# Optimization experiments

Measured on AMD Instinct MI355X. Metric: run time of the kernel, lower is better.

Reference implementation:

```python
import jax, jax.numpy as jnp
import numpy as np

BATCH, N_PRE, N_POST = 1024, 8192, 8192
DT = 0.001
TAU_SYN = 0.005
SYN_NOISE_STD = 0.15
ALPHA_SYN = float(np.exp(-DT / TAU_SYN))  # exp(-dt/tau_syn) decay buffer


def setup_inputs() -> dict:
    key = jax.random.key(0)
    ks = jax.random.split(key, 6)
    spikes = jax.random.uniform(ks[0], (BATCH, N_PRE), dtype=jnp.float32)
    I_syn = jax.random.normal(ks[1], (BATCH, N_POST), dtype=jnp.float32) * 1e-10
    x_std = jax.random.uniform(ks[2], (BATCH, N_PRE), dtype=jnp.float32)
    noise = jax.random.normal(ks[3], (BATCH, N_POST), dtype=jnp.float32)
    # synapse counts from connectome -> norm_counts * mask (precomputed buffer)
    counts = jax.random.randint(ks[4], (N_PRE, N_POST), 0, 8).astype(jnp.float32)
    Wnm = (counts / counts.max()) * (counts > 0).astype(jnp.float32)
    log_strength = jnp.asarray(np.log(5e-09), dtype=jnp.float32)
    log_tau_rec = jnp.asarray(np.log(0.2), dtype=jnp.float32)
    logit_U = jnp.asarray(float(np.log(0.3 / 0.7)), dtype=jnp.float32)  # logit(0.3)
    return {"spikes": spikes, "I_syn": I_syn, "x_std": x_std, "noise": noise,
            "Wnm": Wnm, "log_strength": log_strength,
            "log_tau_rec": log_tau_rec, "logit_U": logit_U}


def reference(spikes, I_syn, x_std, noise, Wnm, log_strength, log_tau_rec, logit_U):
    # effective weights: s * norm_counts * mask  (excitatory sign)
    W = jnp.exp(log_strength) * Wnm                      # (n_pre, n_post)
    # Tsodyks-Markram short-term depression
    tau_rec = jnp.exp(log_tau_rec)
    alpha_rec = jnp.exp(-DT / tau_rec)
    x1 = 1.0 - (1.0 - x_std) * alpha_rec                 # vesicle recovery
    U = jax.nn.sigmoid(logit_U)
    I_inject = jnp.matmul(spikes * U * x1, W)            # (batch, n_post)
    x_new = x1 * (1.0 - U * jnp.clip(spikes, 0.0, 1.0))
    # multiplicative circuit noise
    I_inject = I_inject * (1.0 + noise * SYN_NOISE_STD)
    # exponential synaptic-current decay
    I_syn_new = I_syn * ALPHA_SYN + I_inject
    return I_syn_new, x_new
```

## Files before the change

### kernel.cpp

```cpp
#include <hip/hip_runtime.h>
#include <hip/hip_bf16.h>
#include <cstdint>

#define BATCH 1024
#define NPRE  8192
#define NPOST 8192

typedef _Float16 half8  __attribute__((ext_vector_type(8)));
typedef _Float16 half4_t __attribute__((ext_vector_type(4)));
typedef float    float4_t __attribute__((ext_vector_type(4)));

__device__ constexpr float ALPHA_SYN = 0.8187307530779818f;
__device__ constexpr float DT_C = 0.001f;

__global__ __launch_bounds__(256) void prep_kernel(
    const float* __restrict__ spikes, const float* __restrict__ x_std,
    const float* __restrict__ log_tau_rec, const float* __restrict__ logit_U,
    _Float16* __restrict__ Ah, float* __restrict__ x_new_out)
{
    const float tau_rec   = expf(log_tau_rec[0]);
    const float alpha_rec = expf(-DT_C / tau_rec);
    const float U         = 1.0f / (1.0f + expf(-logit_U[0]));

    const size_t i = ((size_t)blockIdx.x * 256 + threadIdx.x) * 4;
    float4_t sp = *(const float4_t*)(spikes + i);
    float4_t xs = *(const float4_t*)(x_std + i);
    float4_t xn;
    half4_t  a;
#pragma unroll
    for (int j = 0; j < 4; ++j) {
        float x1  = 1.0f - (1.0f - xs[j]) * alpha_rec;
        float av  = sp[j] * U * x1;
        a[j]      = (_Float16)av;
        float spc = fminf(fmaxf(sp[j], 0.0f), 1.0f);
        xn[j]     = x1 * (1.0f - U * spc);
    }
    *(half4_t*)(Ah + i)        = a;
    *(float4_t*)(x_new_out + i) = xn;
}

__global__ __launch_bounds__(256) void transpose_kernel(
    const float* __restrict__ W, _Float16* __restrict__ Wt)
{
    __shared__ float tile[64][65];
    const int n0 = blockIdx.x * 64;
    const int k0 = blockIdx.y * 64;
    const int t  = threadIdx.x;
    const int rr = t >> 4;
    const int cc = t & 15;
#pragma unroll
    for (int it = 0; it < 4; ++it) {
        const int r = it * 16 + rr;
        float4_t v = *(const float4_t*)(W + (size_t)(k0 + r) * NPOST + n0 + cc * 4);
        tile[r][cc * 4 + 0] = v[0];
        tile[r][cc * 4 + 1] = v[1];
        tile[r][cc * 4 + 2] = v[2];
        tile[r][cc * 4 + 3] = v[3];
    }
    __syncthreads();
    const int n  = t >> 2;
    const int kc = (t & 3) * 16;
    half8 h0, h1;
#pragma unroll
    for (int j = 0; j < 8; ++j) h0[j] = (_Float16)tile[kc + j][n];
#pragma unroll
    for (int j = 0; j < 8; ++j) h1[j] = (_Float16)tile[kc + 8 + j][n];
    _Float16* dst = Wt + (size_t)(n0 + n) * NPRE + k0 + kc;
    *(half8*)(dst)     = h0;
    *(half8*)(dst + 8) = h1;
}

#define BM 128
#define BN 128
#define BK 64

__device__ __forceinline__ void gload_lds16(const void* g, void* l) {
    __builtin_amdgcn_global_load_lds(
        (const __attribute__((address_space(1))) void*)g,
        (__attribute__((address_space(3))) void*)l, 16, 0, 0);
}

__global__ __launch_bounds__(256, 2) void gemm_kernel(
    const _Float16* __restrict__ Ah, const _Float16* __restrict__ Wt,
    const float* __restrict__ I_syn, const float* __restrict__ noise,
    const float* __restrict__ log_strength, float* __restrict__ out)
{
    __shared__ _Float16 As[BM * BK];
    __shared__ _Float16 Bs[BN * BK];

    const int tid  = threadIdx.x;
    const int lane = tid & 63;
    const int wid  = tid >> 6;
    const int wr   = wid >> 1;
    const int wc   = wid & 1;
    const int bm0  = blockIdx.y * BM;
    const int bn0  = blockIdx.x * BN;

    const int srow = wid * 32;
    const int r8   = lane >> 3;
    const int c8   = lane & 7;
    const _Float16* ag = Ah + (size_t)(bm0 + srow + r8) * NPRE + c8 * 8;
    const _Float16* bg = Wt + (size_t)(bn0 + srow + r8) * NPRE + c8 * 8;
    _Float16* al = As + srow * BK;
    _Float16* bl = Bs + srow * BK;

    float4_t acc[4][4];
#pragma unroll
    for (int m = 0; m < 4; ++m)
#pragma unroll
        for (int n = 0; n < 4; ++n) acc[m][n] = {0.f, 0.f, 0.f, 0.f};

    const int l16 = lane & 15;
    const int lq  = lane >> 4;

    for (int k0 = 0; k0 < NPRE; k0 += BK) {
#pragma unroll
        for (int i = 0; i < 4; ++i) {
            gload_lds16(ag + (size_t)i * 8 * NPRE + k0, al + i * 8 * BK);
            gload_lds16(bg + (size_t)i * 8 * NPRE + k0, bl + i * 8 * BK);
        }
        __syncthreads();
#pragma unroll
        for (int kk = 0; kk < 2; ++kk) {
            const int koff = kk * 32 + lq * 8;
            half8 af[4], bf[4];
#pragma unroll
            for (int m = 0; m < 4; ++m)
                af[m] = *(const half8*)(As + (wr * 64 + m * 16 + l16) * BK + koff);
#pragma unroll
            for (int n = 0; n < 4; ++n)
                bf[n] = *(const half8*)(Bs + (wc * 64 + n * 16 + l16) * BK + koff);
#pragma unroll
            for (int m = 0; m < 4; ++m)
#pragma unroll
                for (int n = 0; n < 4; ++n)
                    acc[m][n] = __builtin_amdgcn_mfma_f32_16x16x32_f16(
                        af[m], bf[n], acc[m][n], 0, 0, 0);
        }
        __syncthreads();
    }

    const float s = expf(log_strength[0]);
#pragma unroll
    for (int m = 0; m < 4; ++m) {
#pragma unroll
        for (int n = 0; n < 4; ++n) {
            const int col = bn0 + wc * 64 + n * 16 + l16;
#pragma unroll
            for (int r = 0; r < 4; ++r) {
                const int row = bm0 + wr * 64 + m * 16 + lq * 4 + r;
                const size_t idx = (size_t)row * NPOST + col;
                const float inj = acc[m][n][r] * s;
                out[idx] = I_syn[idx] * ALPHA_SYN + inj * (1.0f + noise[idx] * 0.15f);
            }
        }
    }
}

extern "C" void kernel_launch(void* const* d_in, const int* in_sizes, int n_in,
                              void* d_out, int out_size, void* d_ws, size_t ws_size,
                              hipStream_t stream) {
    const float* spikes       = (const float*)d_in[0];
    const float* I_syn        = (const float*)d_in[1];
    const float* x_std        = (const float*)d_in[2];
    const float* noise        = (const float*)d_in[3];
    const float* Wnm          = (const float*)d_in[4];
    const float* log_strength = (const float*)d_in[5];
    const float* log_tau_rec  = (const float*)d_in[6];
    const float* logit_U      = (const float*)d_in[7];
    float* out = (float*)d_out;

    _Float16* Ah = (_Float16*)d_ws;
    _Float16* Wt = (_Float16*)((char*)d_ws + (size_t)BATCH * NPRE * 2);

    float* x_new_out = out + (size_t)BATCH * NPOST;

    prep_kernel<<<(BATCH * NPRE) / (256 * 4), 256, 0, stream>>>(
        spikes, x_std, log_tau_rec, logit_U, Ah, x_new_out);
    transpose_kernel<<<dim3(NPOST / 64, NPRE / 64), 256, 0, stream>>>(Wnm, Wt);
    gemm_kernel<<<dim3(NPOST / BN, BATCH / BM), 256, 0, stream>>>(
        Ah, Wt, I_syn, noise, log_strength, out);
}
```

Baseline: 685.2 us.

## Split-K GEMM with double-buffered LDS and atomic epilogue accumulation

Splits the K dimension of the GEMM in two across a grid z-dimension and accumulates partial results into the output with float atomics. The decayed I_syn term is written ahead of time by the prep kernel. The K tile shrinks to 32 with double-buffered LDS staging so the next tile loads while the current one computes, and launch bounds now target higher occupancy. This trades more parallel blocks and load/compute overlap for extra atomic traffic, a second pass over the noise reads, and a non-deterministic summation order.

```diff
diff --git a/kernel.cpp b/kernel.cpp
--- a/kernel.cpp
+++ b/kernel.cpp
@@ -15,8 +15,9 @@
 
 __global__ __launch_bounds__(256) void prep_kernel(
     const float* __restrict__ spikes, const float* __restrict__ x_std,
+    const float* __restrict__ I_syn,
     const float* __restrict__ log_tau_rec, const float* __restrict__ logit_U,
-    _Float16* __restrict__ Ah, float* __restrict__ x_new_out)
+    _Float16* __restrict__ Ah, float* __restrict__ out)
 {
     const float tau_rec   = expf(log_tau_rec[0]);
     const float alpha_rec = expf(-DT_C / tau_rec);
@@ -25,7 +26,8 @@
     const size_t i = ((size_t)blockIdx.x * 256 + threadIdx.x) * 4;
     float4_t sp = *(const float4_t*)(spikes + i);
     float4_t xs = *(const float4_t*)(x_std + i);
-    float4_t xn;
+    float4_t is = *(const float4_t*)(I_syn + i);
+    float4_t xn, ipre;
     half4_t  a;
 #pragma unroll
     for (int j = 0; j < 4; ++j) {
@@ -34,9 +36,11 @@
         a[j]      = (_Float16)av;
         float spc = fminf(fmaxf(sp[j], 0.0f), 1.0f);
         xn[j]     = x1 * (1.0f - U * spc);
-    }
-    *(half4_t*)(Ah + i)        = a;
-    *(float4_t*)(x_new_out + i) = xn;
+        ipre[j]   = is[j] * ALPHA_SYN;
+    }
+    *(half4_t*)(Ah + i)                          = a;
+    *(float4_t*)(out + (size_t)BATCH * NPOST + i) = xn;
+    *(float4_t*)(out + i)                         = ipre;
 }
 
 __global__ __launch_bounds__(256) void transpose_kernel(
@@ -72,21 +76,23 @@
 
 #define BM 128
 #define BN 128
-#define BK 64
-
-__device__ __forceinline__ void gload_lds16(const void* g, void* l) {
+#define BK 32
+#define SPLITK 2
+#define NT (NPRE / SPLITK / BK)
+
+__device__ __forceinline__ void gload_lds16(const _Float16* g, _Float16* l) {
     __builtin_amdgcn_global_load_lds(
         (const __attribute__((address_space(1))) void*)g,
         (__attribute__((address_space(3))) void*)l, 16, 0, 0);
 }
 
-__global__ __launch_bounds__(256, 2) void gemm_kernel(
+__global__ __launch_bounds__(256, 4) void gemm_kernel(
     const _Float16* __restrict__ Ah, const _Float16* __restrict__ Wt,
-    const float* __restrict__ I_syn, const float* __restrict__ noise,
+    const float* __restrict__ noise,
     const float* __restrict__ log_strength, float* __restrict__ out)
 {
-    __shared__ _Float16 As[BM * BK];
-    __shared__ _Float16 Bs[BN * BK];
+    __shared__ _Float16 As[2][BM * BK];
+    __shared__ _Float16 Bs[2][BN * BK];
 
     const int tid  = threadIdx.x;
     const int lane = tid & 63;
@@ -95,14 +101,12 @@
     const int wc   = wid & 1;
     const int bm0  = blockIdx.y * BM;
     const int bn0  = blockIdx.x * BN;
-
-    const int srow = wid * 32;
-    const int r8   = lane >> 3;
-    const int c8   = lane & 7;
-    const _Float16* ag = Ah + (size_t)(bm0 + srow + r8) * NPRE + c8 * 8;
-    const _Float16* bg = Wt + (size_t)(bn0 + srow + r8) * NPRE + c8 * 8;
-    _Float16* al = As + srow * BK;
-    _Float16* bl = Bs + srow * BK;
+    const int kbase = blockIdx.z * (NPRE / SPLITK);
+
+    const int srow0  = tid >> 2;
+    const int piece  = tid & 3;
+    const _Float16* agb = Ah + (size_t)(bm0 + srow0) * NPRE + kbase + piece * 8;
+    const _Float16* bgb = Wt + (size_t)(bn0 + srow0) * NPRE + kbase + piece * 8;
 
     float4_t acc[4][4];
 #pragma unroll
@@ -113,32 +117,45 @@
     const int l16 = lane & 15;
     const int lq  = lane >> 4;
 
-    for (int k0 = 0; k0 < NPRE; k0 += BK) {
-#pragma unroll
-        for (int i = 0; i < 4; ++i) {
-            gload_lds16(ag + (size_t)i * 8 * NPRE + k0, al + i * 8 * BK);
-            gload_lds16(bg + (size_t)i * 8 * NPRE + k0, bl + i * 8 * BK);
-        }
+#define STAGE(buf, kt)                                                        \
+    {                                                                          \
+        const int kg = (kt) * BK;                                              \
+        _Pragma("unroll")                                                      \
+        for (int j = 0; j < 2; ++j) {                                          \
+            gload_lds16(agb + (size_t)j * 64 * NPRE + kg,                      \
+                        &As[buf][(j * 256 + wid * 64) * 8]);                   \
+            gload_lds16(bgb + (size_t)j * 64 * NPRE + kg,                      \
+                        &Bs[buf][(j * 256 + wid * 64) * 8]);                   \
+        }                                                                      \
+    }
+
+#define COMPUTE(buf)                                                           \
+    {                                                                          \
+        half8 af[4], bf[4];                                                    \
+        _Pragma("unroll")                                                      \
+        for (int m = 0; m < 4; ++m)                                            \
+            af[m] = *(const half8*)&As[buf][(wr * 64 + m * 16 + l16) * BK + lq * 8]; \
+        _Pragma("unroll")                                                      \
+        for (int n = 0; n < 4; ++n)                                            \
+            bf[n] = *(const half8*)&Bs[buf][(wc * 64 + n * 16 + l16) * BK + lq * 8]; \
+        _Pragma("unroll")                                                      \
+        for (int m = 0; m < 4; ++m)                                            \
+            _Pragma("unroll")                                                  \
+            for (int n = 0; n < 4; ++n)                                        \
+                acc[m][n] = __builtin_amdgcn_mfma_f32_16x16x32_f16(            \
+                    af[m], bf[n], acc[m][n], 0, 0, 0);                         \
+    }
+
+    STAGE(0, 0);
+    __syncthreads();
+    int cur = 0;
+    for (int t = 0; t < NT - 1; ++t) {
+        STAGE(cur ^ 1, t + 1);
+        COMPUTE(cur);
         __syncthreads();
-#pragma unroll
-        for (int kk = 0; kk < 2; ++kk) {
-            const int koff = kk * 32 + lq * 8;
-            half8 af[4], bf[4];
-#pragma unroll
-            for (int m = 0; m < 4; ++m)
-                af[m] = *(const half8*)(As + (wr * 64 + m * 16 + l16) * BK + koff);
-#pragma unroll
-            for (int n = 0; n < 4; ++n)
-                bf[n] = *(const half8*)(Bs + (wc * 64 + n * 16 + l16) * BK + koff);
-#pragma unroll
-            for (int m = 0; m < 4; ++m)
-#pragma unroll
-                for (int n = 0; n < 4; ++n)
-                    acc[m][n] = __builtin_amdgcn_mfma_f32_16x16x32_f16(
-                        af[m], bf[n], acc[m][n], 0, 0, 0);
-        }
-        __syncthreads();
-    }
+        cur ^= 1;
+    }
+    COMPUTE(cur);
 
     const float s = expf(log_strength[0]);
 #pragma unroll
@@ -150,11 +167,13 @@
             for (int r = 0; r < 4; ++r) {
                 const int row = bm0 + wr * 64 + m * 16 + lq * 4 + r;
                 const size_t idx = (size_t)row * NPOST + col;
-                const float inj = acc[m][n][r] * s;
-                out[idx] = I_syn[idx] * ALPHA_SYN + inj * (1.0f + noise[idx] * 0.15f);
+                const float v = acc[m][n][r] * s * (1.0f + noise[idx] * 0.15f);
+                unsafeAtomicAdd(&out[idx], v);
             }
         }
     }
+#undef STAGE
+#undef COMPUTE
 }
 
 extern "C" void kernel_launch(void* const* d_in, const int* in_sizes, int n_in,
@@ -173,11 +192,9 @@
     _Float16* Ah = (_Float16*)d_ws;
     _Float16* Wt = (_Float16*)((char*)d_ws + (size_t)BATCH * NPRE * 2);
 
-    float* x_new_out = out + (size_t)BATCH * NPOST;
-
     prep_kernel<<<(BATCH * NPRE) / (256 * 4), 256, 0, stream>>>(
-        spikes, x_std, log_tau_rec, logit_U, Ah, x_new_out);
+        spikes, x_std, I_syn, log_tau_rec, logit_U, Ah, out);
     transpose_kernel<<<dim3(NPOST / 64, NPRE / 64), 256, 0, stream>>>(Wnm, Wt);
-    gemm_kernel<<<dim3(NPOST / BN, BATCH / BM), 256, 0, stream>>>(
-        Ah, Wt, I_syn, noise, log_strength, out);
-}
+    gemm_kernel<<<dim3(NPOST / BN, BATCH / BM, SPLITK), 256, 0, stream>>>(
+        Ah, Wt, noise, log_strength, out);
+}
```

Result: no change. 683.5 us (-0.3%).

## Restructure GEMM with 256x256 tiles, split-K atomics, triple-buffered LDS pipeline

Applied to the files above, without the earlier changes.

The GEMM moves from 128x128 tiles with 256 threads to 256x256 tiles with 512 threads. It uses split-K of 2, and the partial results are combined with atomic adds into an output that prep_kernel pre-initializes with I_syn*alpha. Loads go through a 3-stage LDS ring with explicit vmcnt waits, a swizzled LDS layout to avoid bank conflicts, s_setprio around the MFMA bursts, and XCD-aware block mapping for L2 locality. This aims to raise arithmetic intensity and overlap global loads with MFMA work, at the cost of atomic traffic and a nondeterministic summation order.

```diff
diff --git a/kernel.cpp b/kernel.cpp
--- a/kernel.cpp
+++ b/kernel.cpp
@@ -15,8 +15,9 @@
 
 __global__ __launch_bounds__(256) void prep_kernel(
     const float* __restrict__ spikes, const float* __restrict__ x_std,
+    const float* __restrict__ I_syn,
     const float* __restrict__ log_tau_rec, const float* __restrict__ logit_U,
-    _Float16* __restrict__ Ah, float* __restrict__ x_new_out)
+    _Float16* __restrict__ Ah, float* __restrict__ out)
 {
     const float tau_rec   = expf(log_tau_rec[0]);
     const float alpha_rec = expf(-DT_C / tau_rec);
@@ -25,7 +26,8 @@
     const size_t i = ((size_t)blockIdx.x * 256 + threadIdx.x) * 4;
     float4_t sp = *(const float4_t*)(spikes + i);
     float4_t xs = *(const float4_t*)(x_std + i);
-    float4_t xn;
+    float4_t is = *(const float4_t*)(I_syn + i);
+    float4_t xn, ipre;
     half4_t  a;
 #pragma unroll
     for (int j = 0; j < 4; ++j) {
@@ -34,9 +36,11 @@
         a[j]      = (_Float16)av;
         float spc = fminf(fmaxf(sp[j], 0.0f), 1.0f);
         xn[j]     = x1 * (1.0f - U * spc);
-    }
-    *(half4_t*)(Ah + i)        = a;
-    *(float4_t*)(x_new_out + i) = xn;
+        ipre[j]   = is[j] * ALPHA_SYN;
+    }
+    *(half4_t*)(Ah + i)                           = a;
+    *(float4_t*)(out + (size_t)BATCH * NPOST + i) = xn;
+    *(float4_t*)(out + i)                         = ipre;
 }
 
 __global__ __launch_bounds__(256) void transpose_kernel(
@@ -70,91 +74,141 @@
     *(half8*)(dst + 8) = h1;
 }
 
-#define BM 128
-#define BN 128
-#define BK 64
-
-__device__ __forceinline__ void gload_lds16(const void* g, void* l) {
+#define BM 256
+#define BN 256
+#define BK 32
+#define SPLITK 2
+#define KSPAN (NPRE / SPLITK)
+#define NT (KSPAN / BK)
+
+__device__ __forceinline__ void gload_lds16(const _Float16* g, _Float16* l) {
     __builtin_amdgcn_global_load_lds(
         (const __attribute__((address_space(1))) void*)g,
         (__attribute__((address_space(3))) void*)l, 16, 0, 0);
 }
 
-__global__ __launch_bounds__(256, 2) void gemm_kernel(
+__global__ __launch_bounds__(512, 2) void gemm_kernel(
     const _Float16* __restrict__ Ah, const _Float16* __restrict__ Wt,
-    const float* __restrict__ I_syn, const float* __restrict__ noise,
+    const float* __restrict__ noise,
     const float* __restrict__ log_strength, float* __restrict__ out)
 {
-    __shared__ _Float16 As[BM * BK];
-    __shared__ _Float16 Bs[BN * BK];
+    __shared__ _Float16 As[3][BM * BK];
+    __shared__ _Float16 Bs[3][BN * BK];
 
     const int tid  = threadIdx.x;
     const int lane = tid & 63;
     const int wid  = tid >> 6;
-    const int wr   = wid >> 1;
-    const int wc   = wid & 1;
-    const int bm0  = blockIdx.y * BM;
-    const int bn0  = blockIdx.x * BN;
-
-    const int srow = wid * 32;
-    const int r8   = lane >> 3;
-    const int c8   = lane & 7;
-    const _Float16* ag = Ah + (size_t)(bm0 + srow + r8) * NPRE + c8 * 8;
-    const _Float16* bg = Wt + (size_t)(bn0 + srow + r8) * NPRE + c8 * 8;
-    _Float16* al = As + srow * BK;
-    _Float16* bl = Bs + srow * BK;
-
-    float4_t acc[4][4];
-#pragma unroll
-    for (int m = 0; m < 4; ++m)
-#pragma unroll
-        for (int n = 0; n < 4; ++n) acc[m][n] = {0.f, 0.f, 0.f, 0.f};
+    const int wr   = wid >> 2;
+    const int wc   = wid & 3;
+
+    const int idx   = blockIdx.x;
+    const int xcd   = idx & 7;
+    const int rank  = idx >> 3;
+    const int nblk  = xcd * 4 + (rank & 3);
+    const int mblk  = (rank >> 2) & 3;
+    const int split = rank >> 4;
+    const int bm0   = mblk * BM;
+    const int bn0   = nblk * BN;
+    const int kbase = split * KSPAN;
+
+    const int r0   = wid * 16 + (lane >> 2);
+    const int sl   = lane & 3;
+    const int cswz = (r0 >> 1) & 3;
+    const int pp   = sl ^ cswz;
+    const _Float16* agbase = Ah + (size_t)(bm0 + r0) * NPRE + kbase + pp * 8;
+    const _Float16* bgbase = Wt + (size_t)(bn0 + r0) * NPRE + kbase + pp * 8;
+    const int ldsw = wid * 512;
+
+#define STAGE_A(nb, t)                                                        \
+    {                                                                         \
+        gload_lds16(agbase + (size_t)(t) * BK, &As[nb][ldsw]);                \
+        gload_lds16(agbase + (size_t)128 * NPRE + (size_t)(t) * BK,           \
+                    &As[nb][4096 + ldsw]);                                    \
+    }
+#define STAGE_B(nb, t)                                                        \
+    {                                                                         \
+        gload_lds16(bgbase + (size_t)(t) * BK, &Bs[nb][ldsw]);                \
+        gload_lds16(bgbase + (size_t)128 * NPRE + (size_t)(t) * BK,           \
+                    &Bs[nb][4096 + ldsw]);                                    \
+    }
 
     const int l16 = lane & 15;
     const int lq  = lane >> 4;
-
-    for (int k0 = 0; k0 < NPRE; k0 += BK) {
-#pragma unroll
-        for (int i = 0; i < 4; ++i) {
-            gload_lds16(ag + (size_t)i * 8 * NPRE + k0, al + i * 8 * BK);
-            gload_lds16(bg + (size_t)i * 8 * NPRE + k0, bl + i * 8 * BK);
-        }
-        __syncthreads();
-#pragma unroll
-        for (int kk = 0; kk < 2; ++kk) {
-            const int koff = kk * 32 + lq * 8;
-            half8 af[4], bf[4];
-#pragma unroll
-            for (int m = 0; m < 4; ++m)
-                af[m] = *(const half8*)(As + (wr * 64 + m * 16 + l16) * BK + koff);
+    const int fsw = (lq ^ ((l16 >> 1) & 3)) * 8;
+    int offA0[4], offA1[4], offB[4];
+#pragma unroll
+    for (int m = 0; m < 4; ++m) {
+        offA0[m] = (wr * 128 + m * 16 + l16) * 32 + fsw;
+        offA1[m] = (wr * 128 + (4 + m) * 16 + l16) * 32 + fsw;
+    }
+#pragma unroll
+    for (int n = 0; n < 4; ++n)
+        offB[n] = (wc * 64 + n * 16 + l16) * 32 + fsw;
+
+    float4_t acc[8][4];
+#pragma unroll
+    for (int m = 0; m < 8; ++m)
+#pragma unroll
+        for (int n = 0; n < 4; ++n) acc[m][n] = {0.f, 0.f, 0.f, 0.f};
+
+    STAGE_A(0, 0); STAGE_B(0, 0);
+    STAGE_A(1, 1); STAGE_B(1, 1);
+
+    for (int t = 0; t < NT; ++t) {
+        const int cb = t % 3;
+        const int pb = (t + 2) % 3;
+        if (t < NT - 1) asm volatile("s_waitcnt vmcnt(4)" ::: "memory");
+        else            asm volatile("s_waitcnt vmcnt(0)" ::: "memory");
+        __builtin_amdgcn_s_barrier();
+        const bool pf = (t + 2) < NT;
+
+        if (pf) STAGE_A(pb, t + 2);
+        half8 bf[4], af[4];
+#pragma unroll
+        for (int n = 0; n < 4; ++n) bf[n] = *(const half8*)&Bs[cb][offB[n]];
+#pragma unroll
+        for (int m = 0; m < 4; ++m) af[m] = *(const half8*)&As[cb][offA0[m]];
+        __builtin_amdgcn_s_setprio(1);
+#pragma unroll
+        for (int m = 0; m < 4; ++m)
 #pragma unroll
             for (int n = 0; n < 4; ++n)
-                bf[n] = *(const half8*)(Bs + (wc * 64 + n * 16 + l16) * BK + koff);
-#pragma unroll
-            for (int m = 0; m < 4; ++m)
-#pragma unroll
-                for (int n = 0; n < 4; ++n)
-                    acc[m][n] = __builtin_amdgcn_mfma_f32_16x16x32_f16(
-                        af[m], bf[n], acc[m][n], 0, 0, 0);
-        }
-        __syncthreads();
+                acc[m][n] = __builtin_amdgcn_mfma_f32_16x16x32_f16(
+                    af[m], bf[n], acc[m][n], 0, 0, 0);
+        __builtin_amdgcn_s_setprio(0);
+        __builtin_amdgcn_s_barrier();
+
+        if (pf) STAGE_B(pb, t + 2);
+#pragma unroll
+        for (int m = 0; m < 4; ++m) af[m] = *(const half8*)&As[cb][offA1[m]];
+        __builtin_amdgcn_s_setprio(1);
+#pragma unroll
+        for (int m = 0; m < 4; ++m)
+#pragma unroll
+            for (int n = 0; n < 4; ++n)
+                acc[4 + m][n] = __builtin_amdgcn_mfma_f32_16x16x32_f16(
+                    af[m], bf[n], acc[4 + m][n], 0, 0, 0);
+        __builtin_amdgcn_s_setprio(0);
     }
 
     const float s = expf(log_strength[0]);
-#pragma unroll
-    for (int m = 0; m < 4; ++m) {
+    const int lq4 = lq * 4;
+#pragma unroll
+    for (int m = 0; m < 8; ++m) {
 #pragma unroll
         for (int n = 0; n < 4; ++n) {
             const int col = bn0 + wc * 64 + n * 16 + l16;
 #pragma unroll
             for (int r = 0; r < 4; ++r) {
-                const int row = bm0 + wr * 64 + m * 16 + lq * 4 + r;
-                const size_t idx = (size_t)row * NPOST + col;
-                const float inj = acc[m][n][r] * s;
-                out[idx] = I_syn[idx] * ALPHA_SYN + inj * (1.0f + noise[idx] * 0.15f);
+                const int row = bm0 + wr * 128 + m * 16 + lq4 + r;
+                const size_t o = (size_t)row * NPOST + col;
+                const float v = acc[m][n][r] * s * (1.0f + noise[o] * 0.15f);
+                unsafeAtomicAdd(&out[o], v);
             }
         }
     }
+#undef STAGE_A
+#undef STAGE_B
 }
 
 extern "C" void kernel_launch(void* const* d_in, const int* in_sizes, int n_in,
@@ -173,11 +227,9 @@
     _Float16* Ah = (_Float16*)d_ws;
     _Float16* Wt = (_Float16*)((char*)d_ws + (size_t)BATCH * NPRE * 2);
 
-    float* x_new_out = out + (size_t)BATCH * NPOST;
-
     prep_kernel<<<(BATCH * NPRE) / (256 * 4), 256, 0, stream>>>(
-        spikes, x_std, log_tau_rec, logit_U, Ah, x_new_out);
+        spikes, x_std, I_syn, log_tau_rec, logit_U, Ah, out);
     transpose_kernel<<<dim3(NPOST / 64, NPRE / 64), 256, 0, stream>>>(Wnm, Wt);
-    gemm_kernel<<<dim3(NPOST / BN, BATCH / BM), 256, 0, stream>>>(
-        Ah, Wt, I_syn, noise, log_strength, out);
-}
+    gemm_kernel<<<(NPOST / BN) * (BATCH / BM) * SPLITK, 512, 0, stream>>>(
+        Ah, Wt, noise, log_strength, out);
+}
```

Measured after the change: 704.2 us. 2.8% more time.
